# Optimization experiments

Hardware: AMD Instinct MI355X
Metric: run time of the kernel (lower is better)

Reference implementation:

```python
import jax, jax.numpy as jnp
import numpy as np

B, IN, H, N, W, K = 32, 256, 512, 32768, 64, 8
EPS = 1e-12  # torch F.normalize eps


def setup_inputs() -> dict:
    key = jax.random.key(0)
    ks = jax.random.split(key, 16)
    inp = {
        "x": jax.random.normal(ks[0], (B, IN), jnp.float32),
        "h_prev": jax.random.normal(ks[1], (B, H), jnp.float32),
        "c_prev": jax.random.normal(ks[2], (B, H), jnp.float32),
        "M_prev": jax.random.normal(ks[3], (B, N, W), jnp.float32),
        "wr_prev": jax.random.uniform(ks[4], (B, N), jnp.float32),
        "usage_prev": jax.random.uniform(ks[5], (B, N), jnp.float32),
        "r_prev": jax.random.normal(ks[6], (B, W), jnp.float32),
        # LSTMCell params (torch layout: [4H, in] / [4H, H], gate order i,f,g,o)
        "W_ih": jax.random.normal(ks[7], (4 * H, IN + W), jnp.float32) * 0.02,
        "W_hh": jax.random.normal(ks[8], (4 * H, H), jnp.float32) * 0.02,
        "b_ih": jax.random.normal(ks[9], (4 * H,), jnp.float32) * 0.02,
        "b_hh": jax.random.normal(ks[10], (4 * H,), jnp.float32) * 0.02,
        # output_projector: hidden -> 3W + 2
        "W_proj": jax.random.normal(ks[11], (3 * W + 2, H), jnp.float32) * 0.02,
        "b_proj": jax.random.normal(ks[12], (3 * W + 2,), jnp.float32) * 0.02,
        # final_projector: hidden + W -> hidden
        "W_final": jax.random.normal(ks[13], (H, H + W), jnp.float32) * 0.02,
        "b_final": jax.random.normal(ks[14], (H,), jnp.float32) * 0.02,
    }
    return inp


def _l2norm(v, axis):
    n = jnp.sqrt(jnp.sum(v * v, axis=axis, keepdims=True))
    return v / jnp.maximum(n, EPS)


def reference(x, h_prev, c_prev, M_prev, wr_prev, usage_prev, r_prev,
              W_ih, W_hh, b_ih, b_hh, W_proj, b_proj, W_final, b_final):
    # ---- LSTM controller step ----
    lstm_in = jnp.concatenate([x, r_prev], axis=1)            # [B, IN+W]
    gates = lstm_in @ W_ih.T + b_ih + h_prev @ W_hh.T + b_hh  # [B, 4H]
    gi, gf, gg, go = jnp.split(gates, 4, axis=1)
    i = jax.nn.sigmoid(gi)
    f = jax.nn.sigmoid(gf)
    g = jnp.tanh(gg)
    o = jax.nn.sigmoid(go)
    c_curr = f * c_prev + i * g
    h_curr = o * jnp.tanh(c_curr)

    # ---- interface params ----
    params = h_curr @ W_proj.T + b_proj                       # [B, 3W+2]
    q = params[:, :W]
    a = params[:, W:2 * W]
    e = jax.nn.sigmoid(params[:, 2 * W:3 * W])
    alpha = jax.nn.sigmoid(params[:, -2:-1])                  # [B,1]
    gamma = jax.nn.sigmoid(params[:, -1:])                    # [B,1]

    # ---- sparse read: cosine sim -> topK -> scattered softmax ----
    q_n = _l2norm(q, axis=1)                                  # [B, W]
    m_n = _l2norm(M_prev, axis=2)                             # [B, N, W]
    sim = jnp.einsum('bw,bnw->bn', q_n, m_n)                  # [B, N]
    top_vals, top_idx = jax.lax.top_k(sim, K)                 # [B, K]
    sm = jax.nn.softmax(top_vals, axis=1)                     # softmax(-inf elsewhere) == 0
    b_idx = jnp.arange(sim.shape[0])[:, None]
    w_r = jnp.zeros_like(sim).at[b_idx, top_idx].set(sm)      # [B, N]
    r_curr = jnp.einsum('bn,bnw->bw', w_r, M_prev)            # [B, W]

    # ---- usage / LRU write weights ----
    usage_curr = usage_prev + 1.0
    access_mask = jnp.zeros_like(usage_curr).at[b_idx, top_idx].set(1.0)
    usage_curr = usage_curr * (1.0 - access_mask)
    lru = jnp.argmax(usage_curr, axis=1)                      # [B]
    I_U = jax.nn.one_hot(lru, usage_curr.shape[1], dtype=usage_curr.dtype)
    w_w = alpha * (gamma * wr_prev + (1.0 - gamma) * I_U)     # [B, N]

    # ---- rank-1 erase / add memory update ----
    w_w_exp = w_w[:, :, None]                                 # [B, N, 1]
    M_curr = M_prev * (1.0 - w_w_exp * e[:, None, :]) + w_w_exp * a[:, None, :]

    # ---- output ----
    y_out = jnp.concatenate([h_curr, r_curr], axis=1) @ W_final.T + b_final
    return (y_out, h_curr, c_curr, M_curr, w_r, usage_curr, r_curr)
```

## Files before the change

### kernel.cpp

```cpp
#include <hip/hip_runtime.h>
#include <math.h>

#define B_ 32
#define IN_ 256
#define H_ 512
#define N_ 32768
#define W_ 64
#define K_ 8
#define PROJ_ 194
#define NCHUNK 32
#define CROWS 1024
#define NCAND 1024

typedef float f32x4 __attribute__((ext_vector_type(4)));

#define OUT_Y  0
#define OUT_H  16384
#define OUT_C  32768
#define OUT_M  49152
#define OUT_WR 67158016
#define OUT_US 68206592
#define OUT_R  69255168

#define WS_QN    0
#define WS_AA    2048
#define WS_EE    4096
#define WS_ALPHA 6144
#define WS_GAMMA 6176
#define WS_LRU   6208
#define WS_CVAL  8192
#define WS_CIDX  40960

__device__ __forceinline__ float sigmoidf_(float v) { return 1.f / (1.f + expf(-v)); }

__global__ __launch_bounds__(256) void k_lstm(
    const float* __restrict__ x, const float* __restrict__ r_prev,
    const float* __restrict__ h_prev, const float* __restrict__ c_prev,
    const float* __restrict__ W_ih, const float* __restrict__ W_hh,
    const float* __restrict__ b_ih, const float* __restrict__ b_hh,
    float* __restrict__ h_out, float* __restrict__ c_out) {
  int wid = (blockIdx.x * blockDim.x + threadIdx.x) >> 6;
  int lane = threadIdx.x & 63;
  if (wid >= B_ * H_) return;
  int b = wid >> 9;
  int h = wid & (H_ - 1);
  float a0 = 0.f, a1 = 0.f, a2 = 0.f, a3 = 0.f;
  const float4* x4 = (const float4*)(x + b * IN_);
  const float4* r4 = (const float4*)(r_prev + b * W_);
  for (int c = lane; c < 80; c += 64) {
    float4 in4 = (c < 64) ? x4[c] : r4[c - 64];
    #pragma unroll
    for (int g = 0; g < 4; ++g) {
      float4 w4 = ((const float4*)(W_ih + (size_t)(g * H_ + h) * 320))[c];
      float d = fmaf(w4.x, in4.x, fmaf(w4.y, in4.y, fmaf(w4.z, in4.z, w4.w * in4.w)));
      if (g == 0) a0 += d; else if (g == 1) a1 += d; else if (g == 2) a2 += d; else a3 += d;
    }
  }
  const float4* h4 = (const float4*)(h_prev + b * H_);
  for (int c = lane; c < 128; c += 64) {
    float4 in4 = h4[c];
    #pragma unroll
    for (int g = 0; g < 4; ++g) {
      float4 w4 = ((const float4*)(W_hh + (size_t)(g * H_ + h) * 512))[c];
      float d = fmaf(w4.x, in4.x, fmaf(w4.y, in4.y, fmaf(w4.z, in4.z, w4.w * in4.w)));
      if (g == 0) a0 += d; else if (g == 1) a1 += d; else if (g == 2) a2 += d; else a3 += d;
    }
  }
  #pragma unroll
  for (int m = 1; m < 64; m <<= 1) {
    a0 += __shfl_xor(a0, m); a1 += __shfl_xor(a1, m);
    a2 += __shfl_xor(a2, m); a3 += __shfl_xor(a3, m);
  }
  if (lane == 0) {
    float gi = a0 + b_ih[h] + b_hh[h];
    float gf = a1 + b_ih[H_ + h] + b_hh[H_ + h];
    float gg = a2 + b_ih[2 * H_ + h] + b_hh[2 * H_ + h];
    float go = a3 + b_ih[3 * H_ + h] + b_hh[3 * H_ + h];
    float i_ = sigmoidf_(gi), f_ = sigmoidf_(gf), g_ = tanhf(gg), o_ = sigmoidf_(go);
    float cc = f_ * c_prev[b * H_ + h] + i_ * g_;
    c_out[b * H_ + h] = cc;
    h_out[b * H_ + h] = o_ * tanhf(cc);
  }
}

__global__ __launch_bounds__(256) void k_projpost(
    const float* __restrict__ h_curr, const float* __restrict__ W_proj,
    const float* __restrict__ b_proj, float* __restrict__ qn,
    float* __restrict__ aa, float* __restrict__ ee,
    float* __restrict__ alpha, float* __restrict__ gamma) {
  int b = blockIdx.x, tid = threadIdx.x;
  int wave = tid >> 6, lane = tid & 63;
  __shared__ float params[PROJ_];
  const float4* h4 = (const float4*)(h_curr + b * H_);
  float4 ha = h4[lane], hb = h4[lane + 64];
  for (int p = wave; p < PROJ_; p += 4) {
    const float4* w4p = (const float4*)(W_proj + (size_t)p * H_);
    float4 wa = w4p[lane], wb = w4p[lane + 64];
    float acc = fmaf(wa.x, ha.x, fmaf(wa.y, ha.y, fmaf(wa.z, ha.z, wa.w * ha.w)))
              + fmaf(wb.x, hb.x, fmaf(wb.y, hb.y, fmaf(wb.z, hb.z, wb.w * hb.w)));
    #pragma unroll
    for (int m = 1; m < 64; m <<= 1) acc += __shfl_xor(acc, m);
    if (lane == 0) params[p] = acc + b_proj[p];
  }
  __syncthreads();
  if (tid < W_) {
    float q = params[tid];
    float s = q * q;
    #pragma unroll
    for (int m = 1; m < 64; m <<= 1) s += __shfl_xor(s, m);
    float nrm = fmaxf(sqrtf(s), 1e-12f);
    qn[b * W_ + tid] = q / nrm;
    aa[b * W_ + tid] = params[W_ + tid];
    ee[b * W_ + tid] = sigmoidf_(params[2 * W_ + tid]);
    if (tid == 0) alpha[b] = sigmoidf_(params[192]);
    if (tid == 1) gamma[b] = sigmoidf_(params[193]);
  }
}

#define PROC(mm, ITER) do {                                                   \
    int r_ = (ITER) * 16 + (tid >> 4);                                        \
    float ww_ = wwv[r_];                                                      \
    f32x4 o_;                                                                 \
    o_.x = fmaf(mm.x, 1.f - ww_ * e4.x, ww_ * a4.x);                          \
    o_.y = fmaf(mm.y, 1.f - ww_ * e4.y, ww_ * a4.y);                          \
    o_.z = fmaf(mm.z, 1.f - ww_ * e4.z, ww_ * a4.z);                          \
    o_.w = fmaf(mm.w, 1.f - ww_ * e4.w, ww_ * a4.w);                          \
    Ov[(ITER) * 256 + tid] = o_;                                              \
    float dot_ = fmaf(mm.x, q4.x, fmaf(mm.y, q4.y, fmaf(mm.z, q4.z, mm.w * q4.w))); \
    float sq_  = fmaf(mm.x, mm.x, fmaf(mm.y, mm.y, fmaf(mm.z, mm.z, mm.w * mm.w))); \
    dot_ += __shfl_xor(dot_, 1);  sq_ += __shfl_xor(sq_, 1);                  \
    dot_ += __shfl_xor(dot_, 2);  sq_ += __shfl_xor(sq_, 2);                  \
    dot_ += __shfl_xor(dot_, 4);  sq_ += __shfl_xor(sq_, 4);                  \
    dot_ += __shfl_xor(dot_, 8);  sq_ += __shfl_xor(sq_, 8);                  \
    if (j == 0) simv[r_] = dot_ / fmaxf(sqrtf(sq_), 1e-12f);                  \
  } while (0)

__global__ __launch_bounds__(256, 4) void k_simupd(
    const float* __restrict__ M, const float* __restrict__ qn,
    const float* __restrict__ wr_prev, const float* __restrict__ aa,
    const float* __restrict__ ee, const float* __restrict__ alpha,
    const float* __restrict__ gamma, float* __restrict__ M_out,
    float* __restrict__ cval, int* __restrict__ cidx, float* __restrict__ w_r) {
  int b = blockIdx.y, chunk = blockIdx.x, tid = threadIdx.x;
  int j = tid & 15;
  __shared__ float simv[CROWS];
  __shared__ float wwv[CROWS];
  f32x4 z = {0.f, 0.f, 0.f, 0.f};
  *(f32x4*)(w_r + (size_t)b * N_ + chunk * CROWS + tid * 4) = z;
  const f32x4* Mv = (const f32x4*)(M + ((size_t)b * N_ + (size_t)chunk * CROWS) * W_);
  f32x4* Ov = (f32x4*)(M_out + ((size_t)b * N_ + (size_t)chunk * CROWS) * W_);
  const float* wrb = wr_prev + (size_t)b * N_ + chunk * CROWS;
  float4 q4 = ((const float4*)(qn + b * W_))[j];
  float4 e4 = ((const float4*)(ee + b * W_))[j];
  float4 a4 = ((const float4*)(aa + b * W_))[j];
  float c0 = alpha[b] * gamma[b];
  #pragma unroll
  for (int i = 0; i < 4; ++i) wwv[tid + 256 * i] = c0 * wrb[tid + 256 * i];
  __syncthreads();
  f32x4 bufA[8], bufB[8];
  #pragma unroll
  for (int u = 0; u < 8; ++u) bufA[u] = Mv[u * 256 + tid];
  #pragma unroll
  for (int itb = 0; itb < 64; itb += 16) {
    #pragma unroll
    for (int u = 0; u < 8; ++u) bufB[u] = Mv[(itb + 8 + u) * 256 + tid];
    #pragma unroll
    for (int u = 0; u < 8; ++u) PROC(bufA[u], itb + u);
    if (itb + 16 < 64) {
      #pragma unroll
      for (int u = 0; u < 8; ++u) bufA[u] = Mv[(itb + 16 + u) * 256 + tid];
    }
    #pragma unroll
    for (int u = 0; u < 8; ++u) PROC(bufB[u], itb + 8 + u);
  }
  __syncthreads();
  int wave = tid >> 6, lane = tid & 63;
  int rbase = wave * 256 + lane;
  float v0 = simv[rbase];
  float v1 = simv[rbase + 64];
  float v2 = simv[rbase + 128];
  float v3 = simv[rbase + 192];
  int base = chunk * CROWS + rbase;
  float myv = 0.f; int myi = 0;
  #pragma unroll
  for (int sel = 0; sel < K_; ++sel) {
    float bv = v0; int bk = 0;
    if (v1 > bv) { bv = v1; bk = 1; }
    if (v2 > bv) { bv = v2; bk = 2; }
    if (v3 > bv) { bv = v3; bk = 3; }
    int bi = base + (bk << 6);
    #pragma unroll
    for (int m = 1; m < 64; m <<= 1) {
      float ov = __shfl_xor(bv, m); int oi = __shfl_xor(bi, m);
      if (ov > bv || (ov == bv && oi < bi)) { bv = ov; bi = oi; }
    }
    if (bi == base)            v0 = -INFINITY;
    else if (bi == base + 64)  v1 = -INFINITY;
    else if (bi == base + 128) v2 = -INFINITY;
    else if (bi == base + 192) v3 = -INFINITY;
    if (lane == sel) { myv = bv; myi = bi; }
  }
  if (lane < K_) {
    size_t co = ((size_t)(b * NCHUNK + chunk) * 4 + wave) * K_ + lane;
    cval[co] = myv;
    cidx[co] = myi;
  }
}

__global__ __launch_bounds__(1024) void k_muse(
    const float* __restrict__ cval, const int* __restrict__ cidx,
    const float* __restrict__ M, const float* __restrict__ usage_prev,
    float* __restrict__ usage_out, float* __restrict__ r_out,
    float* __restrict__ w_r, int* __restrict__ lru) {
  int b = blockIdx.x, tid = threadIdx.x;
  __shared__ float wv[16]; __shared__ int wi[16];
  float v = cval[(size_t)b * NCAND + tid];
  int idx = cidx[(size_t)b * NCAND + tid];
  float topv[K_]; int topi[K_];
  #pragma unroll
  for (int sel = 0; sel < K_; ++sel) {
    float bv = v; int bi = idx;
    #pragma unroll
    for (int m = 1; m < 64; m <<= 1) {
      float ov = __shfl_xor(bv, m); int oi = __shfl_xor(bi, m);
      if (ov > bv || (ov == bv && oi < bi)) { bv = ov; bi = oi; }
    }
    if ((tid & 63) == 0) { wv[tid >> 6] = bv; wi[tid >> 6] = bi; }
    __syncthreads();
    float gv = wv[0]; int gi = wi[0];
    #pragma unroll
    for (int w = 1; w < 16; ++w) {
      float ov = wv[w]; int oi = wi[w];
      if (ov > gv || (ov == gv && oi < gi)) { gv = ov; gi = oi; }
    }
    if (idx == gi) v = -INFINITY;
    topv[sel] = gv; topi[sel] = gi;
    __syncthreads();
  }
  float mx = topv[0], ssum = 0.f, e[K_];
  #pragma unroll
  for (int k = 0; k < K_; ++k) { e[k] = expf(topv[k] - mx); ssum += e[k]; }
  #pragma unroll
  for (int k = 0; k < K_; ++k) e[k] /= ssum;
  if (tid < K_) w_r[(size_t)b * N_ + topi[tid]] = e[tid];
  if (tid < W_) {
    float acc = 0.f;
    #pragma unroll
    for (int k = 0; k < K_; ++k)
      acc += e[k] * M[((size_t)b * N_ + (size_t)topi[k]) * W_ + tid];
    r_out[b * W_ + tid] = acc;
  }
  const f32x4* up = (const f32x4*)(usage_prev + (size_t)b * N_);
  f32x4* uo = (f32x4*)(usage_out + (size_t)b * N_);
  float bu = -1.f; int bn = 0x7fffffff;
  for (int i = tid; i < N_ / 4; i += 1024) {
    f32x4 u = up[i];
    int n0 = i * 4;
    float uu[4] = {u.x + 1.f, u.y + 1.f, u.z + 1.f, u.w + 1.f};
    #pragma unroll
    for (int c = 0; c < 4; ++c) {
      int n = n0 + c;
      bool acc = false;
      #pragma unroll
      for (int k = 0; k < K_; ++k) acc |= (n == topi[k]);
      if (acc) uu[c] = 0.f;
      if (uu[c] > bu || (uu[c] == bu && n < bn)) { bu = uu[c]; bn = n; }
    }
    f32x4 w = {uu[0], uu[1], uu[2], uu[3]};
    __builtin_nontemporal_store(w, &uo[i]);
  }
  #pragma unroll
  for (int m = 1; m < 64; m <<= 1) {
    float ov = __shfl_xor(bu, m); int oi = __shfl_xor(bn, m);
    if (ov > bu || (ov == bu && oi < bn)) { bu = ov; bn = oi; }
  }
  if ((tid & 63) == 0) { wv[tid >> 6] = bu; wi[tid >> 6] = bn; }
  __syncthreads();
  if (tid == 0) {
    float gv = wv[0]; int gi = wi[0];
    #pragma unroll
    for (int w = 1; w < 16; ++w) {
      float ov = wv[w]; int oi = wi[w];
      if (ov > gv || (ov == gv && oi < gi)) { gv = ov; gi = oi; }
    }
    lru[b] = gi;
  }
}

__global__ void k_fix(
    const float* __restrict__ M, const float* __restrict__ wr_prev,
    const float* __restrict__ aa, const float* __restrict__ ee,
    const float* __restrict__ alpha, const float* __restrict__ gamma,
    const int* __restrict__ lru, float* __restrict__ M_out) {
  int b = blockIdx.x, t = threadIdx.x;
  int n = lru[b];
  float al = alpha[b], ga = gamma[b];
  float ww = al * (ga * wr_prev[(size_t)b * N_ + n] + (1.f - ga));
  float e = ee[b * W_ + t], a = aa[b * W_ + t];
  float m = M[((size_t)b * N_ + n) * W_ + t];
  M_out[((size_t)b * N_ + n) * W_ + t] = fmaf(m, 1.f - ww * e, ww * a);
}

__global__ __launch_bounds__(256) void k_yout(
    const float* __restrict__ h_curr, const float* __restrict__ r_curr,
    const float* __restrict__ W_final, const float* __restrict__ b_final,
    float* __restrict__ y) {
  int wid = (blockIdx.x * blockDim.x + threadIdx.x) >> 6;
  int lane = threadIdx.x & 63;
  if (wid >= B_ * H_) return;
  int b = wid >> 9;
  int o = wid & (H_ - 1);
  float acc = 0.f;
  const float4* h4 = (const float4*)(h_curr + b * H_);
  const float4* r4 = (const float4*)(r_curr + b * W_);
  const float4* w4p = (const float4*)(W_final + (size_t)o * 576);
  for (int c = lane; c < 144; c += 64) {
    float4 in4 = (c < 128) ? h4[c] : r4[c - 128];
    float4 w4 = w4p[c];
    acc += fmaf(w4.x, in4.x, fmaf(w4.y, in4.y, fmaf(w4.z, in4.z, w4.w * in4.w)));
  }
  #pragma unroll
  for (int m = 1; m < 64; m <<= 1) acc += __shfl_xor(acc, m);
  if (lane == 0) y[b * H_ + o] = acc + b_final[o];
}

extern "C" void kernel_launch(void* const* d_in, const int* in_sizes, int n_in,
                              void* d_out, int out_size, void* d_ws, size_t ws_size,
                              hipStream_t stream) {
  const float* x          = (const float*)d_in[0];
  const float* h_prev     = (const float*)d_in[1];
  const float* c_prev     = (const float*)d_in[2];
  const float* M_prev     = (const float*)d_in[3];
  const float* wr_prev    = (const float*)d_in[4];
  const float* usage_prev = (const float*)d_in[5];
  const float* r_prev     = (const float*)d_in[6];
  const float* W_ih       = (const float*)d_in[7];
  const float* W_hh       = (const float*)d_in[8];
  const float* b_ih       = (const float*)d_in[9];
  const float* b_hh       = (const float*)d_in[10];
  const float* W_proj     = (const float*)d_in[11];
  const float* b_proj     = (const float*)d_in[12];
  const float* W_final    = (const float*)d_in[13];
  const float* b_final    = (const float*)d_in[14];

  float* out   = (float*)d_out;
  float* y_out = out + OUT_Y;
  float* h_out = out + OUT_H;
  float* c_out = out + OUT_C;
  float* M_out = out + OUT_M;
  float* wr_out = out + OUT_WR;
  float* us_out = out + OUT_US;
  float* r_out  = out + OUT_R;

  float* ws    = (float*)d_ws;
  float* qn    = ws + WS_QN;
  float* aa    = ws + WS_AA;
  float* ee    = ws + WS_EE;
  float* alpha = ws + WS_ALPHA;
  float* gamma = ws + WS_GAMMA;
  int*   lru   = (int*)(ws + WS_LRU);
  float* cval  = ws + WS_CVAL;
  int*   cidx  = (int*)(ws + WS_CIDX);

  k_lstm<<<4096, 256, 0, stream>>>(x, r_prev, h_prev, c_prev, W_ih, W_hh, b_ih, b_hh,
                                   h_out, c_out);
  k_projpost<<<32, 256, 0, stream>>>(h_out, W_proj, b_proj, qn, aa, ee, alpha, gamma);
  dim3 sg(NCHUNK, B_);
  k_simupd<<<sg, 256, 0, stream>>>(M_prev, qn, wr_prev, aa, ee, alpha, gamma,
                                   M_out, cval, cidx, wr_out);
  k_muse<<<32, 1024, 0, stream>>>(cval, cidx, M_prev, usage_prev, us_out, r_out,
                                  wr_out, lru);
  k_fix<<<32, 64, 0, stream>>>(M_prev, wr_prev, aa, ee, alpha, gamma, lru, M_out);
  k_yout<<<4096, 256, 0, stream>>>(h_out, r_out, W_final, b_final, y_out);
}
```

Baseline: 206.7 us.

## Warp-specialize similarity/update kernel with LDS ring and dedicated store waves

Doubles the k_simupd block to 512 threads. The first 256 threads load M, compute similarity and the erase/add update, and write the updated rows into one of two shared-memory ring buffers. The other 256 threads drain the previous ring to M_out with nontemporal stores. The aim is to overlap the large global write stream with the loads and compute of the next group. In exchange it adds LDS round trips, a barrier every half-iteration and a larger LDS footprint that may limit occupancy.

```diff
diff --git a/kernel.cpp b/kernel.cpp
--- a/kernel.cpp
+++ b/kernel.cpp
@@ -117,15 +117,15 @@
   }
 }
 
-#define PROC(mm, ITER) do {                                                   \
-    int r_ = (ITER) * 16 + (tid >> 4);                                        \
+#define PROCV(mm, IT, RING) do {                                              \
+    int r_ = (IT) * 16 + (tid >> 4);                                          \
     float ww_ = wwv[r_];                                                      \
     f32x4 o_;                                                                 \
     o_.x = fmaf(mm.x, 1.f - ww_ * e4.x, ww_ * a4.x);                          \
     o_.y = fmaf(mm.y, 1.f - ww_ * e4.y, ww_ * a4.y);                          \
     o_.z = fmaf(mm.z, 1.f - ww_ * e4.z, ww_ * a4.z);                          \
     o_.w = fmaf(mm.w, 1.f - ww_ * e4.w, ww_ * a4.w);                          \
-    Ov[(ITER) * 256 + tid] = o_;                                              \
+    RING[((IT) & 3) * 256 + tid] = o_;                                        \
     float dot_ = fmaf(mm.x, q4.x, fmaf(mm.y, q4.y, fmaf(mm.z, q4.z, mm.w * q4.w))); \
     float sq_  = fmaf(mm.x, mm.x, fmaf(mm.y, mm.y, fmaf(mm.z, mm.z, mm.w * mm.w))); \
     dot_ += __shfl_xor(dot_, 1);  sq_ += __shfl_xor(sq_, 1);                  \
@@ -135,45 +135,98 @@
     if (j == 0) simv[r_] = dot_ / fmaxf(sqrtf(sq_), 1e-12f);                  \
   } while (0)
 
-__global__ __launch_bounds__(256, 4) void k_simupd(
+#define DRAIN(RING, GHALF) do {                                               \
+    int st_ = tid - 256;                                                      \
+    int base_ = (GHALF) * 1024;                                               \
+    f32x4 v0_ = RING[0 * 256 + st_];                                          \
+    f32x4 v1_ = RING[1 * 256 + st_];                                          \
+    f32x4 v2_ = RING[2 * 256 + st_];                                          \
+    f32x4 v3_ = RING[3 * 256 + st_];                                          \
+    __builtin_nontemporal_store(v0_, &Ov[base_ + 0 * 256 + st_]);             \
+    __builtin_nontemporal_store(v1_, &Ov[base_ + 1 * 256 + st_]);             \
+    __builtin_nontemporal_store(v2_, &Ov[base_ + 2 * 256 + st_]);             \
+    __builtin_nontemporal_store(v3_, &Ov[base_ + 3 * 256 + st_]);             \
+  } while (0)
+
+#define LGK_BARRIER() do {                                                    \
+    asm volatile("s_waitcnt lgkmcnt(0)" ::: "memory");                        \
+    __builtin_amdgcn_s_barrier();                                             \
+  } while (0)
+
+__global__ __launch_bounds__(512, 4) void k_simupd(
     const float* __restrict__ M, const float* __restrict__ qn,
     const float* __restrict__ wr_prev, const float* __restrict__ aa,
     const float* __restrict__ ee, const float* __restrict__ alpha,
     const float* __restrict__ gamma, float* __restrict__ M_out,
     float* __restrict__ cval, int* __restrict__ cidx, float* __restrict__ w_r) {
   int b = blockIdx.y, chunk = blockIdx.x, tid = threadIdx.x;
-  int j = tid & 15;
   __shared__ float simv[CROWS];
   __shared__ float wwv[CROWS];
-  f32x4 z = {0.f, 0.f, 0.f, 0.f};
-  *(f32x4*)(w_r + (size_t)b * N_ + chunk * CROWS + tid * 4) = z;
+  __shared__ f32x4 ring0[1024];
+  __shared__ f32x4 ring1[1024];
   const f32x4* Mv = (const f32x4*)(M + ((size_t)b * N_ + (size_t)chunk * CROWS) * W_);
   f32x4* Ov = (f32x4*)(M_out + ((size_t)b * N_ + (size_t)chunk * CROWS) * W_);
-  const float* wrb = wr_prev + (size_t)b * N_ + chunk * CROWS;
-  float4 q4 = ((const float4*)(qn + b * W_))[j];
-  float4 e4 = ((const float4*)(ee + b * W_))[j];
-  float4 a4 = ((const float4*)(aa + b * W_))[j];
-  float c0 = alpha[b] * gamma[b];
-  #pragma unroll
-  for (int i = 0; i < 4; ++i) wwv[tid + 256 * i] = c0 * wrb[tid + 256 * i];
-  __syncthreads();
-  f32x4 bufA[8], bufB[8];
-  #pragma unroll
-  for (int u = 0; u < 8; ++u) bufA[u] = Mv[u * 256 + tid];
-  #pragma unroll
-  for (int itb = 0; itb < 64; itb += 16) {
-    #pragma unroll
-    for (int u = 0; u < 8; ++u) bufB[u] = Mv[(itb + 8 + u) * 256 + tid];
-    #pragma unroll
-    for (int u = 0; u < 8; ++u) PROC(bufA[u], itb + u);
-    if (itb + 16 < 64) {
-      #pragma unroll
-      for (int u = 0; u < 8; ++u) bufA[u] = Mv[(itb + 16 + u) * 256 + tid];
-    }
-    #pragma unroll
-    for (int u = 0; u < 8; ++u) PROC(bufB[u], itb + 8 + u);
-  }
-  __syncthreads();
+
+  int j = tid & 15;
+  float4 q4, e4, a4;
+  f32x4 LA0, LA1, LA2, LA3, LB0, LB1, LB2, LB3;
+
+  if (tid < 256) {
+    const float* wrb = wr_prev + (size_t)b * N_ + chunk * CROWS;
+    q4 = ((const float4*)(qn + b * W_))[j];
+    e4 = ((const float4*)(ee + b * W_))[j];
+    a4 = ((const float4*)(aa + b * W_))[j];
+    float c0 = alpha[b] * gamma[b];
+    #pragma unroll
+    for (int i = 0; i < 4; ++i) wwv[tid + 256 * i] = c0 * wrb[tid + 256 * i];
+    LA0 = Mv[0 * 256 + tid];
+    LA1 = Mv[1 * 256 + tid];
+    LA2 = Mv[2 * 256 + tid];
+    LA3 = Mv[3 * 256 + tid];
+  } else {
+    int st = tid - 256;
+    f32x4 z = {0.f, 0.f, 0.f, 0.f};
+    __builtin_nontemporal_store(z, (f32x4*)(w_r + (size_t)b * N_ + chunk * CROWS + st * 4));
+  }
+  LGK_BARRIER();
+
+  for (int hh = 0; hh < 8; ++hh) {
+    if (tid < 256) {
+      int g1 = 2 * hh + 1;
+      LB0 = Mv[(g1 * 4 + 0) * 256 + tid];
+      LB1 = Mv[(g1 * 4 + 1) * 256 + tid];
+      LB2 = Mv[(g1 * 4 + 2) * 256 + tid];
+      LB3 = Mv[(g1 * 4 + 3) * 256 + tid];
+      PROCV(LA0, 8 * hh + 0, ring0);
+      PROCV(LA1, 8 * hh + 1, ring0);
+      PROCV(LA2, 8 * hh + 2, ring0);
+      PROCV(LA3, 8 * hh + 3, ring0);
+    } else if (hh > 0) {
+      DRAIN(ring1, 2 * hh - 1);
+    }
+    LGK_BARRIER();
+    if (tid < 256) {
+      if (hh < 7) {
+        int g2 = 2 * hh + 2;
+        LA0 = Mv[(g2 * 4 + 0) * 256 + tid];
+        LA1 = Mv[(g2 * 4 + 1) * 256 + tid];
+        LA2 = Mv[(g2 * 4 + 2) * 256 + tid];
+        LA3 = Mv[(g2 * 4 + 3) * 256 + tid];
+      }
+      PROCV(LB0, 8 * hh + 4, ring1);
+      PROCV(LB1, 8 * hh + 5, ring1);
+      PROCV(LB2, 8 * hh + 6, ring1);
+      PROCV(LB3, 8 * hh + 7, ring1);
+    } else {
+      DRAIN(ring0, 2 * hh);
+    }
+    LGK_BARRIER();
+  }
+  if (tid >= 256) {
+    DRAIN(ring1, 15);
+    return;
+  }
+
   int wave = tid >> 6, lane = tid & 63;
   int rbase = wave * 256 + lane;
   float v0 = simv[rbase];
@@ -366,7 +419,7 @@
                                    h_out, c_out);
   k_projpost<<<32, 256, 0, stream>>>(h_out, W_proj, b_proj, qn, aa, ee, alpha, gamma);
   dim3 sg(NCHUNK, B_);
-  k_simupd<<<sg, 256, 0, stream>>>(M_prev, qn, wr_prev, aa, ee, alpha, gamma,
+  k_simupd<<<sg, 512, 0, stream>>>(M_prev, qn, wr_prev, aa, ee, alpha, gamma,
                                    M_out, cval, cidx, wr_out);
   k_muse<<<32, 1024, 0, stream>>>(cval, cidx, M_prev, usage_prev, us_out, r_out,
                                   wr_out, lru);
```

Result: faster. 175.8 us (-15.0%).
